# Optimization experiments

Measured on AMD Instinct MI355X. Metric: run time of the kernel, lower is better.

Reference implementation:

```python
import jax, jax.numpy as jnp
import numpy as np

DIM = 128
NUM_HEADS = 4
HEAD_DIM = DIM // NUM_HEADS
WH, WW = 7, 7
N_TOK = WH * WW
LAMBDA_K = 1.0
TEMP_MAX = 4.0


def _relative_position_index(wh, ww):
    coords = np.stack(np.meshgrid(np.arange(wh), np.arange(ww), indexing='ij'))  # [2,wh,ww]
    flat = coords.reshape(2, -1)                         # [2,N]
    rel = flat[:, :, None] - flat[:, None, :]            # [2,N,N]
    rel = rel.transpose(1, 2, 0).copy()                  # [N,N,2]
    rel[:, :, 0] += wh - 1
    rel[:, :, 1] += ww - 1
    rel[:, :, 0] *= 2 * ww - 1
    return rel.sum(-1).astype(np.int32)                  # [N,N]


def setup_inputs() -> dict:
    key = jax.random.key(0)
    ks = jax.random.split(key, 10)
    B = 4096
    x = jax.random.normal(ks[0], (B, N_TOK, DIM), dtype=jnp.float32)
    token_u_temp = jax.random.normal(ks[1], (B, N_TOK), dtype=jnp.float32)
    token_u_bias = jax.random.normal(ks[2], (B, N_TOK), dtype=jnp.float32)
    token_gate = jax.random.uniform(ks[3], (B, NUM_HEADS, N_TOK), dtype=jnp.float32)
    qkv_w = jax.random.normal(ks[4], (3 * DIM, DIM), dtype=jnp.float32) * (DIM ** -0.5)
    qkv_b = jax.random.normal(ks[5], (3 * DIM,), dtype=jnp.float32) * 0.02
    proj_w = jax.random.normal(ks[6], (DIM, DIM), dtype=jnp.float32) * (DIM ** -0.5)
    proj_b = jax.random.normal(ks[7], (DIM,), dtype=jnp.float32) * 0.02
    rel_table = jax.random.normal(ks[8], ((2 * WH - 1) * (2 * WW - 1), NUM_HEADS), dtype=jnp.float32) * 0.02
    rel_index = jnp.asarray(_relative_position_index(WH, WW))
    return {
        'x': x, 'token_u_temp': token_u_temp, 'token_u_bias': token_u_bias,
        'token_gate': token_gate, 'qkv_w': qkv_w, 'qkv_b': qkv_b,
        'proj_w': proj_w, 'proj_b': proj_b, 'rel_table': rel_table,
        'rel_index': rel_index,
    }


def reference(x, token_u_temp, token_u_bias, token_gate, qkv_w, qkv_b, proj_w, proj_b, rel_table, rel_index):
    B, N, C = x.shape
    qkv = x @ qkv_w.T + qkv_b                             # [B,N,3C]
    qkv = qkv.reshape(B, N, 3, NUM_HEADS, HEAD_DIM).transpose(2, 0, 3, 1, 4)
    q, k, v = qkv[0], qkv[1], qkv[2]                      # [B,H,N,hd]
    # per-token temperature scaling of q
    T = 0.1 + TEMP_MAX * jax.nn.sigmoid(token_u_temp)     # [B,N]
    q = q / T[:, None, :, None]
    # gathered relative-position bias + per-key bias penalty
    bias = rel_table[rel_index.reshape(-1)].reshape(N, N, NUM_HEADS)
    bias = bias.transpose(2, 0, 1)[None]                  # [1,H,N,N]
    uB = jax.nn.relu(token_u_bias)                        # [B,N]
    mask = bias - LAMBDA_K * uB[:, None, None, :]         # [B,H,N,N]
    scores = jnp.einsum('bhnd,bhmd->bhnm', q, k) * (HEAD_DIM ** -0.5) + mask
    attn = jax.nn.softmax(scores, axis=-1)
    out = jnp.einsum('bhnm,bhmd->bhnd', attn, v)          # [B,H,N,hd]
    out = out * token_gate[:, :, :, None]                 # per-token, per-head gate
    out = out.transpose(0, 2, 1, 3).reshape(B, N, C)
    return out @ proj_w.T + proj_b
```

## Files before the change

### kernel.cpp

```cpp
#include <hip/hip_runtime.h>

typedef short s8v __attribute__((ext_vector_type(8)));
typedef float f4v __attribute__((ext_vector_type(4)));

#define NTOK 49
#define LDS_Q    0
#define LDS_K    6468
#define LDS_RT   12936
#define LDS_UB   12985
#define LDS_GATE 13034
#define LDS_TOT  13230

#define WS_BIAS_OFF 262144

__device__ __forceinline__ unsigned short f2bf(float f){
    unsigned x = __float_as_uint(f);
    x += 0x7fffu + ((x >> 16) & 1u);
    return (unsigned short)(x >> 16);
}
__device__ __forceinline__ void split8t(const float* f, s8v& hi, s8v& lo){
    #pragma unroll
    for (int j = 0; j < 8; ++j){
        unsigned u = __float_as_uint(f[j]);
        hi[j] = (short)(u >> 16);
        float r = f[j] - __uint_as_float(u & 0xffff0000u);
        lo[j] = (short)(__float_as_uint(r) >> 16);
    }
}

__global__ void prep_kernel(const float* __restrict__ qkv_w, const float* __restrict__ proj_w,
                            const float* __restrict__ rel_table, const int* __restrict__ rel_index,
                            void* __restrict__ ws){
    int i = blockIdx.x * 256 + threadIdx.x;
    unsigned short* qh = (unsigned short*)ws;
    unsigned short* ql = qh + 49152;
    unsigned short* ph = (unsigned short*)((char*)ws + 196608);
    unsigned short* pl = (unsigned short*)((char*)ws + 229376);
    float* biasT = (float*)((char*)ws + WS_BIAS_OFF);
    if (i < 49152){
        float v = qkv_w[i];
        unsigned u = __float_as_uint(v);
        qh[i] = (unsigned short)(u >> 16);
        ql[i] = (unsigned short)(__float_as_uint(v - __uint_as_float(u & 0xffff0000u)) >> 16);
    } else if (i < 65536){
        int j = i - 49152;
        float v = proj_w[j];
        unsigned u = __float_as_uint(v);
        ph[j] = (unsigned short)(u >> 16);
        pl[j] = (unsigned short)(__float_as_uint(v - __uint_as_float(u & 0xffff0000u)) >> 16);
    } else if (i < 75140){
        int j = i - 65536;
        int h = j / 2401, r = j % 2401;
        biasT[h*2401 + r] = rel_table[rel_index[r]*4 + h];
    }
}

#define MFMA(a,b,c) __builtin_amdgcn_mfma_f32_16x16x32_bf16((a),(b),(c),0,0,0)

__global__ __launch_bounds__(256, 2)
void win_attn(const float* __restrict__ x, const float* __restrict__ u_temp,
              const float* __restrict__ u_bias, const float* __restrict__ gate,
              const float* __restrict__ qkv_b, const float* __restrict__ proj_b,
              const void* __restrict__ ws, float* __restrict__ out)
{
    __shared__ float sm[LDS_TOT];
    const int b = blockIdx.x, tid = threadIdx.x;
    const int l  = tid & 63;
    const int w  = __builtin_amdgcn_readfirstlane(tid >> 6);
    const int lc = l & 15, q4 = l >> 4;

    if (tid < NTOK){
        float u  = u_temp[b*NTOK + tid];
        float sg = 1.f / (1.f + __expf(-u));
        sm[LDS_RT + tid] = 0.17677669529663687f / (0.1f + 4.f*sg);
        float ub = u_bias[b*NTOK + tid];
        sm[LDS_UB + tid] = ub > 0.f ? ub : 0.f;
    }
    if (tid < 196) sm[LDS_GATE + tid] = gate[b*196 + tid];
    __syncthreads();

    const unsigned short* qkh = (const unsigned short*)ws;
    const unsigned short* qkl = qkh + 49152;

    f4v vhold[2][4];
    #pragma unroll
    for (int mp = 0; mp < 2; ++mp){
        s8v ah[2][4], al[2][4];
        #pragma unroll
        for (int m2 = 0; m2 < 2; ++m2){
            int row = (mp*2 + m2)*16 + lc; if (row > 48) row = 48;
            const float* xp = x + ((size_t)b*NTOK + row)*128 + q4*8;
            #pragma unroll
            for (int kf = 0; kf < 4; ++kf){
                float xv[8];
                float4 t0 = *(const float4*)(xp + kf*32);
                float4 t1 = *(const float4*)(xp + kf*32 + 4);
                xv[0]=t0.x; xv[1]=t0.y; xv[2]=t0.z; xv[3]=t0.w;
                xv[4]=t1.x; xv[5]=t1.y; xv[6]=t1.z; xv[7]=t1.w;
                split8t(xv, ah[m2][kf], al[m2][kf]);
            }
        }
        #pragma unroll
        for (int g = 0; g < 3; ++g){
            #pragma unroll
            for (int t = 0; t < 2; ++t){
                int nt  = (g==0 ? 2*w : (g==1 ? 8+2*w : 16+2*w)) + t;
                int col = nt*16 + lc;
                s8v bh[4], bl[4];
                #pragma unroll
                for (int kf = 0; kf < 4; ++kf){
                    int off = col*128 + kf*32 + q4*8;
                    bh[kf] = *(const s8v*)(qkh + off);
                    bl[kf] = *(const s8v*)(qkl + off);
                }
                float bia = qkv_b[col];
                #pragma unroll
                for (int m2 = 0; m2 < 2; ++m2){
                    f4v acc = {bia, bia, bia, bia};
                    #pragma unroll
                    for (int kf = 0; kf < 4; ++kf){
                        acc = MFMA(ah[m2][kf], bh[kf], acc);
                        acc = MFMA(ah[m2][kf], bl[kf], acc);
                        acc = MFMA(al[m2][kf], bh[kf], acc);
                    }
                    int mt = mp*2 + m2;
                    if (g == 2){
                        vhold[t][mt] = acc;
                    } else {
                        #pragma unroll
                        for (int r = 0; r < 4; ++r){
                            int row = mt*16 + q4*4 + r;
                            if (row < NTOK){
                                if (g == 0) sm[LDS_Q + row*132 + col] = acc[r] * sm[LDS_RT + row];
                                else        sm[LDS_K + row*132 + (col - 128)] = acc[r];
                            }
                        }
                    }
                }
            }
        }
    }

    s8v Kh[4], Kl[4], Qh[4], Ql[4];
    #pragma unroll
    for (int t = 0; t < 4; ++t){
        int row = 16*t + lc; if (row > 48) row = 48;
        float fv[8];
        {
            const float* p = &sm[LDS_K + row*132 + w*32 + q4*8];
            float4 a0 = *(const float4*)p; float4 a1 = *(const float4*)(p + 4);
            fv[0]=a0.x; fv[1]=a0.y; fv[2]=a0.z; fv[3]=a0.w;
            fv[4]=a1.x; fv[5]=a1.y; fv[6]=a1.z; fv[7]=a1.w;
            split8t(fv, Kh[t], Kl[t]);
        }
        {
            const float* p = &sm[LDS_Q + row*132 + w*32 + q4*8];
            float4 a0 = *(const float4*)p; float4 a1 = *(const float4*)(p + 4);
            fv[0]=a0.x; fv[1]=a0.y; fv[2]=a0.z; fv[3]=a0.w;
            fv[4]=a1.x; fv[5]=a1.y; fv[6]=a1.z; fv[7]=a1.w;
            split8t(fv, Qh[t], Ql[t]);
        }
    }
    const float* biasT = (const float*)((const char*)ws + WS_BIAS_OFF);
    f4v S[4][4];
    #pragma unroll
    for (int mt = 0; mt < 4; ++mt){
        #pragma unroll
        for (int nt = 0; nt < 4; ++nt){
            int qy = nt*16 + lc; if (qy > 48) qy = 48;
            f4v a;
            #pragma unroll
            for (int r = 0; r < 4; ++r){
                int ky = mt*16 + q4*4 + r; if (ky > 48) ky = 48;
                a[r] = biasT[w*2401 + qy*49 + ky] - sm[LDS_UB + ky];
            }
            a = MFMA(Kh[mt], Qh[nt], a);
            a = MFMA(Kh[mt], Ql[nt], a);
            a = MFMA(Kl[mt], Qh[nt], a);
            S[mt][nt] = a;
        }
    }
    #pragma unroll
    for (int r = 0; r < 4; ++r){
        int ky = 48 + q4*4 + r;
        if (ky >= NTOK){
            S[3][0][r] = -1e30f; S[3][1][r] = -1e30f; S[3][2][r] = -1e30f; S[3][3][r] = -1e30f;
        }
    }
    #pragma unroll
    for (int nt = 0; nt < 4; ++nt){
        float mx = -3e38f;
        #pragma unroll
        for (int mt = 0; mt < 4; ++mt)
            #pragma unroll
            for (int r = 0; r < 4; ++r) mx = fmaxf(mx, S[mt][nt][r]);
        mx = fmaxf(mx, __shfl_xor(mx, 16));
        mx = fmaxf(mx, __shfl_xor(mx, 32));
        float sum = 0.f;
        #pragma unroll
        for (int mt = 0; mt < 4; ++mt)
            #pragma unroll
            for (int r = 0; r < 4; ++r){
                float e = __expf(S[mt][nt][r] - mx);
                S[mt][nt][r] = e; sum += e;
            }
        sum += __shfl_xor(sum, 16);
        sum += __shfl_xor(sum, 32);
        float rs = 1.f / sum;
        #pragma unroll
        for (int mt = 0; mt < 4; ++mt)
            #pragma unroll
            for (int r = 0; r < 4; ++r) S[mt][nt][r] *= rs;
    }

    unsigned short* P = (unsigned short*)sm;
    #pragma unroll
    for (int nt = 0; nt < 4; ++nt){
        int qy = nt*16 + lc;
        if (qy < NTOK){
            #pragma unroll
            for (int mt = 0; mt < 4; ++mt)
                #pragma unroll
                for (int r = 0; r < 4; ++r){
                    int ky = mt*16 + q4*4 + r;
                    P[(qy*132 + w*32)*2 + (((ky>>3) ^ (qy&7)) << 3) + (ky&7)] = f2bf(S[mt][nt][r]);
                }
        }
    }
    #pragma unroll
    for (int t = 0; t < 2; ++t)
        #pragma unroll
        for (int mt = 0; mt < 4; ++mt)
            #pragma unroll
            for (int r = 0; r < 4; ++r){
                int row = mt*16 + q4*4 + r;
                if (row < NTOK) sm[LDS_K + row*132 + w*32 + t*16 + lc] = vhold[t][mt][r];
            }

    s8v Pa[4][2];
    #pragma unroll
    for (int mt = 0; mt < 4; ++mt)
        #pragma unroll
        for (int kf = 0; kf < 2; ++kf){
            int qy = mt*16 + lc; if (qy > 48) qy = 48;
            int ch = (4*kf + q4) ^ (qy & 7);
            Pa[mt][kf] = *(const s8v*)(P + (qy*132 + w*32)*2 + ch*8);
        }
    s8v Vb[2][2];
    #pragma unroll
    for (int t = 0; t < 2; ++t)
        #pragma unroll
        for (int kf = 0; kf < 2; ++kf){
            #pragma unroll
            for (int j = 0; j < 8; ++j){
                int key = kf*32 + q4*8 + j; if (key > 48) key = 48;
                Vb[t][kf][j] = (short)(__float_as_uint(sm[LDS_K + key*132 + w*32 + t*16 + lc]) >> 16);
            }
        }
    f4v O[4][2];
    #pragma unroll
    for (int mt = 0; mt < 4; ++mt)
        #pragma unroll
        for (int t = 0; t < 2; ++t){
            f4v o = {0.f, 0.f, 0.f, 0.f};
            o = MFMA(Pa[mt][0], Vb[t][0], o);
            o = MFMA(Pa[mt][1], Vb[t][1], o);
            O[mt][t] = o;
        }

    #pragma unroll
    for (int mt = 0; mt < 4; ++mt)
        #pragma unroll
        for (int t = 0; t < 2; ++t)
            #pragma unroll
            for (int r = 0; r < 4; ++r){
                int row = mt*16 + q4*4 + r;
                if (row < NTOK){
                    float vg = O[mt][t][r] * sm[LDS_GATE + w*49 + row];
                    unsigned u = __float_as_uint(vg);
                    float res = vg - __uint_as_float(u & 0xffff0000u);
                    char* bp = (char*)sm + (LDS_K + row*132 + w*32)*4;
                    ((unsigned short*)bp)[t*16 + lc]        = (unsigned short)(u >> 16);
                    ((unsigned short*)(bp + 64))[t*16 + lc] = (unsigned short)(__float_as_uint(res) >> 16);
                }
            }
    __syncthreads();

    const unsigned short* ph = (const unsigned short*)((const char*)ws + 196608);
    const unsigned short* pl = (const unsigned short*)((const char*)ws + 229376);
    s8v Bh[2][4], Bl[2][4];
    #pragma unroll
    for (int t = 0; t < 2; ++t){
        int col = (2*w + t)*16 + lc;
        #pragma unroll
        for (int kf = 0; kf < 4; ++kf){
            int off = col*128 + kf*32 + q4*8;
            Bh[t][kf] = *(const s8v*)(ph + off);
            Bl[t][kf] = *(const s8v*)(pl + off);
        }
    }
    #pragma unroll
    for (int mt = 0; mt < 4; ++mt){
        int row = mt*16 + lc; if (row > 48) row = 48;
        s8v Ah[4], Al[4];
        #pragma unroll
        for (int kf = 0; kf < 4; ++kf){
            const char* bp = (const char*)sm + (LDS_K + row*132 + kf*32)*4;
            Ah[kf] = *(const s8v*)(bp + q4*16);
            Al[kf] = *(const s8v*)(bp + 64 + q4*16);
        }
        #pragma unroll
        for (int t = 0; t < 2; ++t){
            int col = (2*w + t)*16 + lc;
            float bia = proj_b[col];
            f4v acc = {bia, bia, bia, bia};
            #pragma unroll
            for (int kf = 0; kf < 4; ++kf){
                acc = MFMA(Ah[kf], Bh[t][kf], acc);
                acc = MFMA(Ah[kf], Bl[t][kf], acc);
                acc = MFMA(Al[kf], Bh[t][kf], acc);
            }
            #pragma unroll
            for (int r = 0; r < 4; ++r){
                int r2 = mt*16 + q4*4 + r;
                if (r2 < NTOK) out[((size_t)b*NTOK + r2)*128 + col] = acc[r];
            }
        }
    }
}

extern "C" void kernel_launch(void* const* d_in, const int* in_sizes, int n_in,
                              void* d_out, int out_size, void* d_ws, size_t ws_size,
                              hipStream_t stream) {
    const float* x  = (const float*)d_in[0];
    const float* ut = (const float*)d_in[1];
    const float* ub = (const float*)d_in[2];
    const float* tg = (const float*)d_in[3];
    const float* qw = (const float*)d_in[4];
    const float* qb = (const float*)d_in[5];
    const float* pw = (const float*)d_in[6];
    const float* pb = (const float*)d_in[7];
    const float* rt = (const float*)d_in[8];
    const int*   ri = (const int*)d_in[9];
    float* o = (float*)d_out;
    const int B = in_sizes[0] / (NTOK * 128);

    prep_kernel<<<294, 256, 0, stream>>>(qw, pw, rt, ri, d_ws);
    win_attn<<<B, 256, 0, stream>>>(x, ut, ub, tg, qb, pb, d_ws, o);
}
```

Baseline: 451.4 us.

## Compute V, Q, K in separate passes through one LDS buffer to raise occupancy

The QKV projection is split into three passes (V, then Q, then K), each writing to a single shared LDS region and converting into per-wave bf16 registers before the next pass overwrites it. This halves LDS use, drops the V register hold, and computes and normalises the softmax one query tile at a time, so launch bounds move from 2 to 4 blocks per CU. In exchange, x is reloaded and re-split three times. Correctness now depends on each wave touching only its own 32-column head slice between the reduced barriers.

```diff
diff --git a/kernel.cpp b/kernel.cpp
--- a/kernel.cpp
+++ b/kernel.cpp
@@ -4,12 +4,10 @@
 typedef float f4v __attribute__((ext_vector_type(4)));
 
 #define NTOK 49
-#define LDS_Q    0
-#define LDS_K    6468
-#define LDS_RT   12936
-#define LDS_UB   12985
-#define LDS_GATE 13034
-#define LDS_TOT  13230
+#define LDS_RT   6468
+#define LDS_UB   6517
+#define LDS_GATE 6566
+#define LDS_TOT  6762
 
 #define WS_BIAS_OFF 262144
 
@@ -57,7 +55,64 @@
 
 #define MFMA(a,b,c) __builtin_amdgcn_mfma_f32_16x16x32_bf16((a),(b),(c),0,0,0)
 
-__global__ __launch_bounds__(256, 2)
+__device__ __forceinline__ void qkv_pass(const float* __restrict__ x,
+        const unsigned short* __restrict__ qkh, const unsigned short* __restrict__ qkl,
+        const float* __restrict__ qkv_b, float* sm,
+        int b, int w, int lc, int q4, int gbase, bool scaleq)
+{
+    #pragma unroll
+    for (int mp = 0; mp < 2; ++mp){
+        s8v ah[2][4], al[2][4];
+        #pragma unroll
+        for (int m2 = 0; m2 < 2; ++m2){
+            int row = (mp*2 + m2)*16 + lc; if (row > 48) row = 48;
+            const float* xp = x + ((size_t)b*NTOK + row)*128 + q4*8;
+            #pragma unroll
+            for (int kf = 0; kf < 4; ++kf){
+                float xv[8];
+                float4 t0 = *(const float4*)(xp + kf*32);
+                float4 t1 = *(const float4*)(xp + kf*32 + 4);
+                xv[0]=t0.x; xv[1]=t0.y; xv[2]=t0.z; xv[3]=t0.w;
+                xv[4]=t1.x; xv[5]=t1.y; xv[6]=t1.z; xv[7]=t1.w;
+                split8t(xv, ah[m2][kf], al[m2][kf]);
+            }
+        }
+        #pragma unroll
+        for (int t = 0; t < 2; ++t){
+            int col = (gbase + 2*w + t)*16 + lc;
+            float bia = qkv_b[col];
+            f4v acc0 = {bia, bia, bia, bia};
+            f4v acc1 = {bia, bia, bia, bia};
+            #pragma unroll
+            for (int kf = 0; kf < 4; ++kf){
+                int off = col*128 + kf*32 + q4*8;
+                s8v bh = *(const s8v*)(qkh + off);
+                s8v bl = *(const s8v*)(qkl + off);
+                acc0 = MFMA(ah[0][kf], bh, acc0);
+                acc0 = MFMA(ah[0][kf], bl, acc0);
+                acc0 = MFMA(al[0][kf], bh, acc0);
+                acc1 = MFMA(ah[1][kf], bh, acc1);
+                acc1 = MFMA(ah[1][kf], bl, acc1);
+                acc1 = MFMA(al[1][kf], bh, acc1);
+            }
+            #pragma unroll
+            for (int m2 = 0; m2 < 2; ++m2){
+                f4v acc = m2 ? acc1 : acc0;
+                #pragma unroll
+                for (int r = 0; r < 4; ++r){
+                    int row = (mp*2 + m2)*16 + q4*4 + r;
+                    if (row < NTOK){
+                        float v = acc[r];
+                        if (scaleq) v *= sm[LDS_RT + row];
+                        sm[row*132 + w*32 + t*16 + lc] = v;
+                    }
+                }
+            }
+        }
+    }
+}
+
+__global__ __launch_bounds__(256, 4)
 void win_attn(const float* __restrict__ x, const float* __restrict__ u_temp,
               const float* __restrict__ u_bias, const float* __restrict__ gate,
               const float* __restrict__ qkv_b, const float* __restrict__ proj_b,
@@ -77,123 +132,80 @@
         sm[LDS_UB + tid] = ub > 0.f ? ub : 0.f;
     }
     if (tid < 196) sm[LDS_GATE + tid] = gate[b*196 + tid];
-    __syncthreads();
 
     const unsigned short* qkh = (const unsigned short*)ws;
     const unsigned short* qkl = qkh + 49152;
 
-    f4v vhold[2][4];
-    #pragma unroll
-    for (int mp = 0; mp < 2; ++mp){
-        s8v ah[2][4], al[2][4];
-        #pragma unroll
-        for (int m2 = 0; m2 < 2; ++m2){
-            int row = (mp*2 + m2)*16 + lc; if (row > 48) row = 48;
-            const float* xp = x + ((size_t)b*NTOK + row)*128 + q4*8;
-            #pragma unroll
-            for (int kf = 0; kf < 4; ++kf){
-                float xv[8];
-                float4 t0 = *(const float4*)(xp + kf*32);
-                float4 t1 = *(const float4*)(xp + kf*32 + 4);
-                xv[0]=t0.x; xv[1]=t0.y; xv[2]=t0.z; xv[3]=t0.w;
-                xv[4]=t1.x; xv[5]=t1.y; xv[6]=t1.z; xv[7]=t1.w;
-                split8t(xv, ah[m2][kf], al[m2][kf]);
-            }
-        }
-        #pragma unroll
-        for (int g = 0; g < 3; ++g){
-            #pragma unroll
-            for (int t = 0; t < 2; ++t){
-                int nt  = (g==0 ? 2*w : (g==1 ? 8+2*w : 16+2*w)) + t;
-                int col = nt*16 + lc;
-                s8v bh[4], bl[4];
-                #pragma unroll
-                for (int kf = 0; kf < 4; ++kf){
-                    int off = col*128 + kf*32 + q4*8;
-                    bh[kf] = *(const s8v*)(qkh + off);
-                    bl[kf] = *(const s8v*)(qkl + off);
-                }
-                float bia = qkv_b[col];
-                #pragma unroll
-                for (int m2 = 0; m2 < 2; ++m2){
-                    f4v acc = {bia, bia, bia, bia};
-                    #pragma unroll
-                    for (int kf = 0; kf < 4; ++kf){
-                        acc = MFMA(ah[m2][kf], bh[kf], acc);
-                        acc = MFMA(ah[m2][kf], bl[kf], acc);
-                        acc = MFMA(al[m2][kf], bh[kf], acc);
-                    }
-                    int mt = mp*2 + m2;
-                    if (g == 2){
-                        vhold[t][mt] = acc;
-                    } else {
-                        #pragma unroll
-                        for (int r = 0; r < 4; ++r){
-                            int row = mt*16 + q4*4 + r;
-                            if (row < NTOK){
-                                if (g == 0) sm[LDS_Q + row*132 + col] = acc[r] * sm[LDS_RT + row];
-                                else        sm[LDS_K + row*132 + (col - 128)] = acc[r];
-                            }
-                        }
-                    }
-                }
-            }
-        }
-    }
-
-    s8v Kh[4], Kl[4], Qh[4], Ql[4];
+    qkv_pass(x, qkh, qkl, qkv_b, sm, b, w, lc, q4, 16, false);
+    s8v Vb[2][2];
+    #pragma unroll
+    for (int t = 0; t < 2; ++t)
+        #pragma unroll
+        for (int kf = 0; kf < 2; ++kf)
+            #pragma unroll
+            for (int j = 0; j < 8; ++j){
+                int key = kf*32 + q4*8 + j; if (key > 48) key = 48;
+                Vb[t][kf][j] = (short)(__float_as_uint(sm[key*132 + w*32 + t*16 + lc]) >> 16);
+            }
+
+    __syncthreads();
+
+    qkv_pass(x, qkh, qkl, qkv_b, sm, b, w, lc, q4, 0, true);
+    s8v Qh[4], Ql[4];
     #pragma unroll
     for (int t = 0; t < 4; ++t){
         int row = 16*t + lc; if (row > 48) row = 48;
+        const float* p = &sm[row*132 + w*32 + q4*8];
         float fv[8];
-        {
-            const float* p = &sm[LDS_K + row*132 + w*32 + q4*8];
-            float4 a0 = *(const float4*)p; float4 a1 = *(const float4*)(p + 4);
-            fv[0]=a0.x; fv[1]=a0.y; fv[2]=a0.z; fv[3]=a0.w;
-            fv[4]=a1.x; fv[5]=a1.y; fv[6]=a1.z; fv[7]=a1.w;
-            split8t(fv, Kh[t], Kl[t]);
-        }
-        {
-            const float* p = &sm[LDS_Q + row*132 + w*32 + q4*8];
-            float4 a0 = *(const float4*)p; float4 a1 = *(const float4*)(p + 4);
-            fv[0]=a0.x; fv[1]=a0.y; fv[2]=a0.z; fv[3]=a0.w;
-            fv[4]=a1.x; fv[5]=a1.y; fv[6]=a1.z; fv[7]=a1.w;
-            split8t(fv, Qh[t], Ql[t]);
-        }
-    }
+        float4 a0 = *(const float4*)p; float4 a1 = *(const float4*)(p + 4);
+        fv[0]=a0.x; fv[1]=a0.y; fv[2]=a0.z; fv[3]=a0.w;
+        fv[4]=a1.x; fv[5]=a1.y; fv[6]=a1.z; fv[7]=a1.w;
+        split8t(fv, Qh[t], Ql[t]);
+    }
+
+    qkv_pass(x, qkh, qkl, qkv_b, sm, b, w, lc, q4, 8, false);
+    s8v Kh[4], Kl[4];
+    #pragma unroll
+    for (int t = 0; t < 4; ++t){
+        int row = 16*t + lc; if (row > 48) row = 48;
+        const float* p = &sm[row*132 + w*32 + q4*8];
+        float fv[8];
+        float4 a0 = *(const float4*)p; float4 a1 = *(const float4*)(p + 4);
+        fv[0]=a0.x; fv[1]=a0.y; fv[2]=a0.z; fv[3]=a0.w;
+        fv[4]=a1.x; fv[5]=a1.y; fv[6]=a1.z; fv[7]=a1.w;
+        split8t(fv, Kh[t], Kl[t]);
+    }
+
     const float* biasT = (const float*)((const char*)ws + WS_BIAS_OFF);
-    f4v S[4][4];
-    #pragma unroll
-    for (int mt = 0; mt < 4; ++mt){
-        #pragma unroll
-        for (int nt = 0; nt < 4; ++nt){
-            int qy = nt*16 + lc; if (qy > 48) qy = 48;
+    unsigned short* P = (unsigned short*)sm;
+    #pragma unroll
+    for (int nt = 0; nt < 4; ++nt){
+        int qy = nt*16 + lc;
+        int qyc = qy > 48 ? 48 : qy;
+        f4v S[4];
+        #pragma unroll
+        for (int mt = 0; mt < 4; ++mt){
             f4v a;
             #pragma unroll
             for (int r = 0; r < 4; ++r){
                 int ky = mt*16 + q4*4 + r; if (ky > 48) ky = 48;
-                a[r] = biasT[w*2401 + qy*49 + ky] - sm[LDS_UB + ky];
+                a[r] = biasT[w*2401 + qyc*49 + ky] - sm[LDS_UB + ky];
             }
             a = MFMA(Kh[mt], Qh[nt], a);
             a = MFMA(Kh[mt], Ql[nt], a);
             a = MFMA(Kl[mt], Qh[nt], a);
-            S[mt][nt] = a;
-        }
-    }
-    #pragma unroll
-    for (int r = 0; r < 4; ++r){
-        int ky = 48 + q4*4 + r;
-        if (ky >= NTOK){
-            S[3][0][r] = -1e30f; S[3][1][r] = -1e30f; S[3][2][r] = -1e30f; S[3][3][r] = -1e30f;
-        }
-    }
-    #pragma unroll
-    for (int nt = 0; nt < 4; ++nt){
+            S[mt] = a;
+        }
+        #pragma unroll
+        for (int r = 0; r < 4; ++r){
+            int ky = 48 + q4*4 + r;
+            if (ky >= NTOK) S[3][r] = -1e30f;
+        }
         float mx = -3e38f;
         #pragma unroll
         for (int mt = 0; mt < 4; ++mt)
             #pragma unroll
-            for (int r = 0; r < 4; ++r) mx = fmaxf(mx, S[mt][nt][r]);
+            for (int r = 0; r < 4; ++r) mx = fmaxf(mx, S[mt][r]);
         mx = fmaxf(mx, __shfl_xor(mx, 16));
         mx = fmaxf(mx, __shfl_xor(mx, 32));
         float sum = 0.f;
@@ -201,41 +213,22 @@
         for (int mt = 0; mt < 4; ++mt)
             #pragma unroll
             for (int r = 0; r < 4; ++r){
-                float e = __expf(S[mt][nt][r] - mx);
-                S[mt][nt][r] = e; sum += e;
+                float e = __expf(S[mt][r] - mx);
+                S[mt][r] = e; sum += e;
             }
         sum += __shfl_xor(sum, 16);
         sum += __shfl_xor(sum, 32);
         float rs = 1.f / sum;
-        #pragma unroll
-        for (int mt = 0; mt < 4; ++mt)
-            #pragma unroll
-            for (int r = 0; r < 4; ++r) S[mt][nt][r] *= rs;
-    }
-
-    unsigned short* P = (unsigned short*)sm;
-    #pragma unroll
-    for (int nt = 0; nt < 4; ++nt){
-        int qy = nt*16 + lc;
         if (qy < NTOK){
             #pragma unroll
             for (int mt = 0; mt < 4; ++mt)
                 #pragma unroll
                 for (int r = 0; r < 4; ++r){
                     int ky = mt*16 + q4*4 + r;
-                    P[(qy*132 + w*32)*2 + (((ky>>3) ^ (qy&7)) << 3) + (ky&7)] = f2bf(S[mt][nt][r]);
+                    P[(qy*132 + w*32)*2 + (((ky>>3) ^ (qy&7)) << 3) + (ky&7)] = f2bf(S[mt][r] * rs);
                 }
         }
     }
-    #pragma unroll
-    for (int t = 0; t < 2; ++t)
-        #pragma unroll
-        for (int mt = 0; mt < 4; ++mt)
-            #pragma unroll
-            for (int r = 0; r < 4; ++r){
-                int row = mt*16 + q4*4 + r;
-                if (row < NTOK) sm[LDS_K + row*132 + w*32 + t*16 + lc] = vhold[t][mt][r];
-            }
 
     s8v Pa[4][2];
     #pragma unroll
@@ -245,17 +238,6 @@
             int qy = mt*16 + lc; if (qy > 48) qy = 48;
             int ch = (4*kf + q4) ^ (qy & 7);
             Pa[mt][kf] = *(const s8v*)(P + (qy*132 + w*32)*2 + ch*8);
-        }
-    s8v Vb[2][2];
-    #pragma unroll
-    for (int t = 0; t < 2; ++t)
-        #pragma unroll
-        for (int kf = 0; kf < 2; ++kf){
-            #pragma unroll
-            for (int j = 0; j < 8; ++j){
-                int key = kf*32 + q4*8 + j; if (key > 48) key = 48;
-                Vb[t][kf][j] = (short)(__float_as_uint(sm[LDS_K + key*132 + w*32 + t*16 + lc]) >> 16);
-            }
         }
     f4v O[4][2];
     #pragma unroll
@@ -279,7 +261,7 @@
                     float vg = O[mt][t][r] * sm[LDS_GATE + w*49 + row];
                     unsigned u = __float_as_uint(vg);
                     float res = vg - __uint_as_float(u & 0xffff0000u);
-                    char* bp = (char*)sm + (LDS_K + row*132 + w*32)*4;
+                    char* bp = (char*)sm + (row*132 + w*32)*4;
                     ((unsigned short*)bp)[t*16 + lc]        = (unsigned short)(u >> 16);
                     ((unsigned short*)(bp + 64))[t*16 + lc] = (unsigned short)(__float_as_uint(res) >> 16);
                 }
@@ -305,7 +287,7 @@
         s8v Ah[4], Al[4];
         #pragma unroll
         for (int kf = 0; kf < 4; ++kf){
-            const char* bp = (const char*)sm + (LDS_K + row*132 + kf*32)*4;
+            const char* bp = (const char*)sm + (row*132 + kf*32)*4;
             Ah[kf] = *(const s8v*)(bp + q4*16);
             Al[kf] = *(const s8v*)(bp + 64 + q4*16);
         }
```

Result: slower. 753.9 us (+67.0%).
